# Kernel optimization log

Hardware: AMD Instinct MI355X
Metric: run time of the kernel (lower is better)

Reference implementation:

```python
import jax, jax.numpy as jnp
import numpy as np

E, B, C, M, H = 8, 2, 1024, 2048, 7168


def setup_inputs() -> dict:
    key = jax.random.key(0)
    k1, k2, k3, k4 = jax.random.split(key, 4)
    # kaiming_uniform-ish scale for weights (bound = sqrt(6/fan_in)/sqrt(1+5) ~ 1/sqrt(fan_in))
    s_in = 1.0 / np.sqrt(M)
    s_ffn = 1.0 / np.sqrt(H)
    return {
        "dispatch_input": jax.random.normal(k1, (E, B, C, M), dtype=jnp.float32),
        "w1": jax.random.uniform(k2, (E, M, H), dtype=jnp.float32, minval=-s_in, maxval=s_in),
        "w2": jax.random.uniform(k3, (E, H, M), dtype=jnp.float32, minval=-s_ffn, maxval=s_ffn),
        "w3": jax.random.uniform(k4, (E, M, H), dtype=jnp.float32, minval=-s_in, maxval=s_in),
    }


def reference(dispatch_input, w1, w2, w3):
    # Batched per-expert SwiGLU MLP.
    # gate: [E,B,C,H], up: [E,B,C,H]
    gate = jnp.einsum("ebcm,emh->ebch", dispatch_input, w1)
    up = jnp.einsum("ebcm,emh->ebch", dispatch_input, w3)
    hidden = jax.nn.silu(gate) * up
    out = jnp.einsum("ebch,ehm->ebcm", hidden, w2)
    return out
```

## Files before the change

kernel.cpp:

```cpp
#include <hip/hip_runtime.h>

typedef __attribute__((ext_vector_type(8))) short bf16x8;
typedef __attribute__((ext_vector_type(4))) float f32x4;
typedef __attribute__((ext_vector_type(4))) unsigned int u32x4;
typedef __attribute__((ext_vector_type(4))) unsigned short u16x4;

#define NE 8
#define NT 2048
#define NM 2048
#define NH 7168

#define BAR() asm volatile("s_barrier" ::: "memory")
#define WAITV(N) asm volatile("s_waitcnt vmcnt(" #N ")" ::: "memory")

__device__ __forceinline__ unsigned short f2bf(float f) {
    unsigned int u = __float_as_uint(f);
    return (unsigned short)((u + 0x7fffu + ((u >> 16) & 1u)) >> 16);
}

__device__ __forceinline__ void gld16(const void* g, void* l) {
    __builtin_amdgcn_global_load_lds(
        (const __attribute__((address_space(1))) void*)g,
        (__attribute__((address_space(3))) void*)l, 16, 0, 0);
}


__global__ __launch_bounds__(256) void convert_x_kernel(
        const float* __restrict__ in, unsigned short* __restrict__ out) {
    const int i = blockIdx.x * 256 + threadIdx.x;
    f32x4 a = ((const f32x4*)in)[i];
    ((u16x4*)out)[i] = (u16x4){f2bf(a[0]), f2bf(a[1]), f2bf(a[2]), f2bf(a[3])};
}

__global__ __launch_bounds__(256) void convert_wT_kernel(
        const float* __restrict__ in, unsigned short* __restrict__ out,
        int R, int C) {
    const int t = threadIdx.x;
    const int e = blockIdx.y;
    const int tiles_c = C >> 6;
    const int tr = blockIdx.x / tiles_c, tc = blockIdx.x % tiles_c;

    const float* ip = in + (size_t)e * R * C + (size_t)(tr * 64) * C + tc * 64;
    unsigned short* op = out + (size_t)e * R * C + (size_t)(tc * 64) * R + tr * 64;

    __shared__ unsigned short tl[64][68];

    const int rr = t >> 4, c4 = (t & 15) * 4;
#pragma unroll
    for (int q = 0; q < 4; ++q) {
        const int r = q * 16 + rr;
        f32x4 v = *(const f32x4*)(ip + (size_t)r * C + c4);
        *(u16x4*)&tl[r][c4] = (u16x4){f2bf(v[0]), f2bf(v[1]), f2bf(v[2]), f2bf(v[3])};
    }
    __syncthreads();
#pragma unroll
    for (int q = 0; q < 4; ++q) {
        const int oc = q * 16 + rr;
        u16x4 v = (u16x4){tl[c4][oc], tl[c4 + 1][oc], tl[c4 + 2][oc], tl[c4 + 3][oc]};
        *(u16x4*)(op + (size_t)oc * R + c4) = v;
    }
}

__global__ __launch_bounds__(256) void convert_w13_kernel(
        const float* __restrict__ w1, const float* __restrict__ w3,
        unsigned short* __restrict__ wcat) {
    const int t = threadIdx.x;
    const int e = blockIdx.y;
    const int tiles_c = NH >> 6;
    const int tr = blockIdx.x / tiles_c, tc = blockIdx.x % tiles_c;

    __shared__ unsigned short tl[64][68];
    const int rr = t >> 4, c4 = (t & 15) * 4;
    unsigned short* ob = wcat + (size_t)e * (2 * NH) * NM + (size_t)(tc * 128) * NM + tr * 64;

#pragma unroll
    for (int pass = 0; pass < 2; ++pass) {
        const float* ip = (pass ? w3 : w1) + (size_t)e * NM * NH + (size_t)(tr * 64) * NH + tc * 64;
        if (pass) __syncthreads();
#pragma unroll
        for (int q = 0; q < 4; ++q) {
            const int r = q * 16 + rr;
            f32x4 v = *(const f32x4*)(ip + (size_t)r * NH + c4);
            *(u16x4*)&tl[r][c4] = (u16x4){f2bf(v[0]), f2bf(v[1]), f2bf(v[2]), f2bf(v[3])};
        }
        __syncthreads();
#pragma unroll
        for (int q = 0; q < 4; ++q) {
            const int oc = q * 16 + rr;
            const int orow = ((oc >> 4) * 32) + pass * 16 + (oc & 15);
            u16x4 v = (u16x4){tl[c4][oc], tl[c4 + 1][oc], tl[c4 + 2][oc], tl[c4 + 3][oc]};
            *(u16x4*)(ob + (size_t)orow * NM + c4) = v;
        }
    }
}

__global__ __launch_bounds__(512, 2) void gemm1p_kernel(
        const unsigned short* __restrict__ xb, const unsigned short* __restrict__ wcat,
        unsigned short* __restrict__ hid) {
    const int tid = threadIdx.x;
    const int lane = tid & 63, wv = tid >> 6;
    const int wr = wv >> 2, wc = wv & 3;
    const int e = blockIdx.y;
    const int d = blockIdx.x;
    const int l = (d & 7) * 56 + (d >> 3);
    const int ct = l >> 3, tt = l & 7;

    const unsigned short* ag = xb   + (size_t)(e * NT + tt * 256) * NM;
    const unsigned short* bg = wcat + (size_t)e * (2 * NH) * NM + (size_t)(ct * 256) * NM;
    unsigned short* hg = hid + (size_t)(e * NT + tt * 256) * NH + ct * 128;

    __shared__ __align__(16) unsigned short lds[2 * 16384];

    const int frow = lane & 15;
    const int fks  = (lane >> 4) * 8;
    const int la   = lane * 8;
    const int lr   = lane & 15, lq = lane >> 4;

    f32x4 acc[8][4];
#pragma unroll
    for (int m = 0; m < 8; ++m)
#pragma unroll
        for (int n = 0; n < 4; ++n) acc[m][n] = (f32x4){0.f, 0.f, 0.f, 0.f};

    auto stageA = [&](int t, int buf) {
        unsigned short* dst = lds + buf * 16384 + wv * 512;
        const unsigned short* src = ag + (size_t)(wv * 16 + frow) * NM + t * 32 + fks;
        gld16(src, dst);
        gld16(src + (size_t)128 * NM, dst + 8 * 512);
    };
    auto stageB = [&](int t, int buf) {
        unsigned short* dst = lds + buf * 16384 + 8192 + wv * 512;
        const unsigned short* src = bg + (size_t)(wv * 16 + frow) * NM + t * 32 + fks;
        gld16(src, dst);
        gld16(src + (size_t)128 * NM, dst + 8 * 512);
    };

    auto body = [&](int buf) {
        const unsigned short* bA = lds + buf * 16384;
        const unsigned short* bB = bA + 8192;
        bf16x8 af[4], bf[4];
#pragma unroll
        for (int m = 0; m < 4; ++m)
            af[m] = *(const bf16x8*)(bA + (wr * 8 + m) * 512 + la);
#pragma unroll
        for (int n = 0; n < 4; ++n)
            bf[n] = *(const bf16x8*)(bB + (wc * 4 + n) * 512 + la);
        __builtin_amdgcn_s_setprio(1);
#pragma unroll
        for (int m = 0; m < 4; ++m)
#pragma unroll
            for (int n = 0; n < 4; ++n)
                acc[m][n] = __builtin_amdgcn_mfma_f32_16x16x32_bf16(af[m], bf[n], acc[m][n], 0, 0, 0);
        __builtin_amdgcn_s_setprio(0);
#pragma unroll
        for (int m = 0; m < 4; ++m)
            af[m] = *(const bf16x8*)(bA + (wr * 8 + 4 + m) * 512 + la);
        __builtin_amdgcn_s_setprio(1);
#pragma unroll
        for (int m = 0; m < 4; ++m)
#pragma unroll
            for (int n = 0; n < 4; ++n)
                acc[4 + m][n] = __builtin_amdgcn_mfma_f32_16x16x32_bf16(af[m], bf[n], acc[4 + m][n], 0, 0, 0);
        __builtin_amdgcn_s_setprio(0);
    };

    const int NKT = NM / 32;
    stageA(0, 0); stageB(0, 0);

    int buf = 0;
    for (int t = 0; t < NKT; ++t) {
        if (t + 1 < NKT) {
            stageA(t + 1, buf ^ 1);
            stageB(t + 1, buf ^ 1);
            WAITV(4);
        } else {
            WAITV(0);
        }
        BAR();
        body(buf);
        BAR();
        buf ^= 1;
    }

#pragma unroll
    for (int mf = 0; mf < 8; ++mf)
#pragma unroll
        for (int p = 0; p < 2; ++p)
#pragma unroll
            for (int i = 0; i < 4; ++i) {
                const float g = acc[mf][2 * p][i];
                const float u = acc[mf][2 * p + 1][i];
                const float s = g / (1.f + __expf(-g));
                const int r = wr * 128 + mf * 16 + lq * 4 + i;
                const int h = wc * 32 + p * 16 + lr;
                hg[(size_t)r * NH + h] = f2bf(s * u);
            }
}

__global__ __launch_bounds__(512, 2) void gemm2p_kernel(
        const unsigned short* __restrict__ hid, const unsigned short* __restrict__ w2t,
        float* __restrict__ out) {
    const int tid = threadIdx.x;
    const int lane = tid & 63, wv = tid >> 6;
    const int wr = wv >> 2, wc = wv & 3;
    const int e = blockIdx.y;
    const int d = blockIdx.x;
    const int l = (d & 7) * 8 + (d >> 3);
    const int mt = l >> 3, tt = l & 7;

    const unsigned short* ag = hid + (size_t)(e * NT + tt * 256) * NH;
    const unsigned short* bg = w2t + (size_t)e * NM * NH + (size_t)(mt * 256) * NH;
    float* og = out + (size_t)(e * NT + tt * 256) * NM + mt * 256;

    __shared__ __align__(16) unsigned short lds[2 * 16384];

    const int frow = lane & 15;
    const int fks  = (lane >> 4) * 8;
    const int la   = lane * 8;
    const int lr   = lane & 15, lq = lane >> 4;

    f32x4 acc[8][4];
#pragma unroll
    for (int m = 0; m < 8; ++m)
#pragma unroll
        for (int n = 0; n < 4; ++n) acc[m][n] = (f32x4){0.f, 0.f, 0.f, 0.f};

    auto stageA = [&](int t, int buf) {
        unsigned short* dst = lds + buf * 16384 + wv * 512;
        const unsigned short* src = ag + (size_t)(wv * 16 + frow) * NH + t * 32 + fks;
        gld16(src, dst);
        gld16(src + (size_t)128 * NH, dst + 8 * 512);
    };
    auto stageB = [&](int t, int buf) {
        unsigned short* dst = lds + buf * 16384 + 8192 + wv * 512;
        const unsigned short* src = bg + (size_t)(wv * 16 + frow) * NH + t * 32 + fks;
        gld16(src, dst);
        gld16(src + (size_t)128 * NH, dst + 8 * 512);
    };

    auto body = [&](int buf) {
        const unsigned short* bA = lds + buf * 16384;
        const unsigned short* bB = bA + 8192;
        bf16x8 af[4], bf[4];
#pragma unroll
        for (int m = 0; m < 4; ++m)
            af[m] = *(const bf16x8*)(bA + (wr * 8 + m) * 512 + la);
#pragma unroll
        for (int n = 0; n < 4; ++n)
            bf[n] = *(const bf16x8*)(bB + (wc * 4 + n) * 512 + la);
        __builtin_amdgcn_s_setprio(1);
#pragma unroll
        for (int m = 0; m < 4; ++m)
#pragma unroll
            for (int n = 0; n < 4; ++n)
                acc[m][n] = __builtin_amdgcn_mfma_f32_16x16x32_bf16(af[m], bf[n], acc[m][n], 0, 0, 0);
        __builtin_amdgcn_s_setprio(0);
#pragma unroll
        for (int m = 0; m < 4; ++m)
            af[m] = *(const bf16x8*)(bA + (wr * 8 + 4 + m) * 512 + la);
        __builtin_amdgcn_s_setprio(1);
#pragma unroll
        for (int m = 0; m < 4; ++m)
#pragma unroll
            for (int n = 0; n < 4; ++n)
                acc[4 + m][n] = __builtin_amdgcn_mfma_f32_16x16x32_bf16(af[m], bf[n], acc[4 + m][n], 0, 0, 0);
        __builtin_amdgcn_s_setprio(0);
    };

    const int NKT = NH / 32;
    stageA(0, 0); stageB(0, 0);

    int buf = 0;
    for (int t = 0; t < NKT; ++t) {
        if (t + 1 < NKT) {
            stageA(t + 1, buf ^ 1);
            stageB(t + 1, buf ^ 1);
            WAITV(4);
        } else {
            WAITV(0);
        }
        BAR();
        body(buf);
        BAR();
        buf ^= 1;
    }

#pragma unroll
    for (int mf = 0; mf < 8; ++mf)
#pragma unroll
        for (int n = 0; n < 4; ++n)
#pragma unroll
            for (int i = 0; i < 4; ++i) {
                const int r = wr * 128 + mf * 16 + lq * 4 + i;
                const int c = wc * 64 + n * 16 + lr;
                og[(size_t)r * NM + c] = acc[mf][n][i];
            }
}

#define ROWB 80
#define TILEB (128 * ROWB)

__global__ __launch_bounds__(256, 2) void gemm1_fb_kernel(
        const float* __restrict__ x, const float* __restrict__ w1,
        const float* __restrict__ w3, unsigned short* __restrict__ hid) {
    const int tid = threadIdx.x;
    const int e = blockIdx.y;
    const int d = blockIdx.x;
    const int l = (d & 7) * 112 + (d >> 3);
    const int hn = l >> 4, tm = l & 15;

    const float* xg  = x  + (size_t)(e * NT + tm * 128) * NM;
    const float* w1g = w1 + (size_t)e * NM * NH + hn * 128;
    const float* w3g = w3 + (size_t)e * NM * NH + hn * 128;
    unsigned short* hg = hid + (size_t)(e * NT + tm * 128) * NH + hn * 128;

    __shared__ __align__(16) unsigned char lds[2 * 3 * TILEB];

    const int a_r = tid >> 3, a_c4 = tid & 7;
    const int w_kq = (tid >> 2) & 7;
    const int w_cg = ((tid >> 5) << 2) | (tid & 3);

    const int lane = tid & 63;
    const int wv = tid >> 6;
    const int r0w = (wv >> 1) * 64, c0w = (wv & 1) * 64;
    const int lr = lane & 15, lq = lane >> 4;

    f32x4 accg[4][4], accu[4][4];
#pragma unroll
    for (int m = 0; m < 4; ++m)
#pragma unroll
        for (int n = 0; n < 4; ++n) {
            accg[m][n] = (f32x4){0.f, 0.f, 0.f, 0.f};
            accu[m][n] = (f32x4){0.f, 0.f, 0.f, 0.f};
        }

    f32x4 la0, la1, la2, la3;
    f32x4 l10, l11, l12, l13, l30, l31, l32, l33;

    auto stage_load = [&](int ks) {
        const int k0 = ks * 32;
        const float* pa = xg + (size_t)a_r * NM + k0 + a_c4 * 4;
        la0 = *(const f32x4*)(pa);
        la1 = *(const f32x4*)(pa + 32 * NM);
        la2 = *(const f32x4*)(pa + 64 * NM);
        la3 = *(const f32x4*)(pa + 96 * NM);
        const float* p1 = w1g + (size_t)(k0 + w_kq * 4) * NH + w_cg * 4;
        l10 = *(const f32x4*)(p1);
        l11 = *(const f32x4*)(p1 + NH);
        l12 = *(const f32x4*)(p1 + 2 * NH);
        l13 = *(const f32x4*)(p1 + 3 * NH);
        const float* p3 = w3g + (size_t)(k0 + w_kq * 4) * NH + w_cg * 4;
        l30 = *(const f32x4*)(p3);
        l31 = *(const f32x4*)(p3 + NH);
        l32 = *(const f32x4*)(p3 + 2 * NH);
        l33 = *(const f32x4*)(p3 + 3 * NH);
    };

    auto stage_write = [&](int buf) {
        unsigned char* base = lds + buf * (3 * TILEB);
        unsigned char* pa = base + a_r * ROWB + a_c4 * 8;
        *(u16x4*)(pa)             = (u16x4){f2bf(la0[0]), f2bf(la0[1]), f2bf(la0[2]), f2bf(la0[3])};
        *(u16x4*)(pa + 32 * ROWB) = (u16x4){f2bf(la1[0]), f2bf(la1[1]), f2bf(la1[2]), f2bf(la1[3])};
        *(u16x4*)(pa + 64 * ROWB) = (u16x4){f2bf(la2[0]), f2bf(la2[1]), f2bf(la2[2]), f2bf(la2[3])};
        *(u16x4*)(pa + 96 * ROWB) = (u16x4){f2bf(la3[0]), f2bf(la3[1]), f2bf(la3[2]), f2bf(la3[3])};
        unsigned char* pw1 = base + TILEB + w_kq * 8;
#pragma unroll
        for (int j = 0; j < 4; ++j) {
            const int c = w_cg * 4 + j;
            *(u16x4*)(pw1 + c * ROWB) =
                (u16x4){f2bf(l10[j]), f2bf(l11[j]), f2bf(l12[j]), f2bf(l13[j])};
        }
        unsigned char* pw3 = base + 2 * TILEB + w_kq * 8;
#pragma unroll
        for (int j = 0; j < 4; ++j) {
            const int c = w_cg * 4 + j;
            *(u16x4*)(pw3 + c * ROWB) =
                (u16x4){f2bf(l30[j]), f2bf(l31[j]), f2bf(l32[j]), f2bf(l33[j])};
        }
    };

    auto compute = [&](int buf) {
        const unsigned char* base = lds + buf * (3 * TILEB);
        bf16x8 af[4], b1f[4], b3f[4];
#pragma unroll
        for (int m = 0; m < 4; ++m)
            af[m] = *(const bf16x8*)(base + (r0w + m * 16 + lr) * ROWB + lq * 16);
#pragma unroll
        for (int n = 0; n < 4; ++n) {
            b1f[n] = *(const bf16x8*)(base + TILEB + (c0w + n * 16 + lr) * ROWB + lq * 16);
            b3f[n] = *(const bf16x8*)(base + 2 * TILEB + (c0w + n * 16 + lr) * ROWB + lq * 16);
        }
#pragma unroll
        for (int m = 0; m < 4; ++m)
#pragma unroll
            for (int n = 0; n < 4; ++n) {
                accg[m][n] = __builtin_amdgcn_mfma_f32_16x16x32_bf16(af[m], b1f[n], accg[m][n], 0, 0, 0);
                accu[m][n] = __builtin_amdgcn_mfma_f32_16x16x32_bf16(af[m], b3f[n], accu[m][n], 0, 0, 0);
            }
    };

    stage_load(0);
    stage_write(0);
    __syncthreads();
    int cur = 0;
    const int NK = NM / 32;
    for (int ks = 0; ks < NK; ++ks) {
        const bool more = (ks + 1 < NK);
        if (more) stage_load(ks + 1);
        compute(cur);
        if (more) {
            stage_write(cur ^ 1);
            __syncthreads();
        }
        cur ^= 1;
    }

#pragma unroll
    for (int m = 0; m < 4; ++m)
#pragma unroll
        for (int n = 0; n < 4; ++n)
#pragma unroll
            for (int i = 0; i < 4; ++i) {
                const float g = accg[m][n][i];
                const float u = accu[m][n][i];
                const float s = g / (1.f + __expf(-g));
                const int r = r0w + m * 16 + lq * 4 + i;
                const int c = c0w + n * 16 + lr;
                hg[(size_t)r * NH + c] = f2bf(s * u);
            }
}

__global__ __launch_bounds__(256, 2) void gemm2_fb_kernel(
        const unsigned short* __restrict__ hid, const float* __restrict__ w2,
        float* __restrict__ out) {
    const int tid = threadIdx.x;
    const int e = blockIdx.y;
    const int d = blockIdx.x;
    const int l = (d & 7) * 32 + (d >> 3);
    const int mn = l >> 4, tm = l & 15;

    const unsigned short* ag = hid + (size_t)(e * NT + tm * 128) * NH;
    const float* wg = w2 + (size_t)e * NH * NM + mn * 128;
    float* og = out + (size_t)(e * NT + tm * 128) * NM + mn * 128;

    __shared__ __align__(16) unsigned char lds[2 * 2 * TILEB];

    const int a_row = tid >> 2, a_ch = tid & 3;
    const int w_kq = (tid >> 2) & 7;
    const int w_cg = ((tid >> 5) << 2) | (tid & 3);

    const int lane = tid & 63;
    const int wv = tid >> 6;
    const int r0w = (wv >> 1) * 64, c0w = (wv & 1) * 64;
    const int lr = lane & 15, lq = lane >> 4;

    f32x4 acc[4][4];
#pragma unroll
    for (int m = 0; m < 4; ++m)
#pragma unroll
        for (int n = 0; n < 4; ++n) acc[m][n] = (f32x4){0.f, 0.f, 0.f, 0.f};

    u32x4 lau0, lau1;
    f32x4 lw0, lw1, lw2, lw3;

    auto stage_load = [&](int ks) {
        const int k0 = ks * 32;
        lau0 = *(const u32x4*)(ag + (size_t)a_row * NH + k0 + a_ch * 8);
        lau1 = *(const u32x4*)(ag + (size_t)(a_row + 64) * NH + k0 + a_ch * 8);
        const float* p = wg + (size_t)(k0 + w_kq * 4) * NM + w_cg * 4;
        lw0 = *(const f32x4*)(p);
        lw1 = *(const f32x4*)(p + NM);
        lw2 = *(const f32x4*)(p + 2 * NM);
        lw3 = *(const f32x4*)(p + 3 * NM);
    };

    auto stage_write = [&](int buf) {
        unsigned char* base = lds + buf * (2 * TILEB);
        *(u32x4*)(base + a_row * ROWB + a_ch * 16) = lau0;
        *(u32x4*)(base + (a_row + 64) * ROWB + a_ch * 16) = lau1;
        unsigned char* pw = base + TILEB + w_kq * 8;
#pragma unroll
        for (int j = 0; j < 4; ++j) {
            const int c = w_cg * 4 + j;
            *(u16x4*)(pw + c * ROWB) =
                (u16x4){f2bf(lw0[j]), f2bf(lw1[j]), f2bf(lw2[j]), f2bf(lw3[j])};
        }
    };

    auto compute = [&](int buf) {
        const unsigned char* base = lds + buf * (2 * TILEB);
        bf16x8 af[4], bf[4];
#pragma unroll
        for (int m = 0; m < 4; ++m)
            af[m] = *(const bf16x8*)(base + (r0w + m * 16 + lr) * ROWB + lq * 16);
#pragma unroll
        for (int n = 0; n < 4; ++n)
            bf[n] = *(const bf16x8*)(base + TILEB + (c0w + n * 16 + lr) * ROWB + lq * 16);
#pragma unroll
        for (int m = 0; m < 4; ++m)
#pragma unroll
            for (int n = 0; n < 4; ++n)
                acc[m][n] = __builtin_amdgcn_mfma_f32_16x16x32_bf16(af[m], bf[n], acc[m][n], 0, 0, 0);
    };

    stage_load(0);
    stage_write(0);
    __syncthreads();
    int cur = 0;
    const int NK = NH / 32;
    for (int ks = 0; ks < NK; ++ks) {
        const bool more = (ks + 1 < NK);
        if (more) stage_load(ks + 1);
        compute(cur);
        if (more) {
            stage_write(cur ^ 1);
            __syncthreads();
        }
        cur ^= 1;
    }

#pragma unroll
    for (int m = 0; m < 4; ++m)
#pragma unroll
        for (int n = 0; n < 4; ++n)
#pragma unroll
            for (int i = 0; i < 4; ++i) {
                const int r = r0w + m * 16 + lq * 4 + i;
                const int c = c0w + n * 16 + lr;
                og[(size_t)r * NM + c] = acc[m][n][i];
            }
}


extern "C" void kernel_launch(void* const* d_in, const int* in_sizes, int n_in,
                              void* d_out, int out_size, void* d_ws, size_t ws_size,
                              hipStream_t stream) {
    const float* x  = (const float*)d_in[0];
    const float* w1 = (const float*)d_in[1];
    const float* w2 = (const float*)d_in[2];
    const float* w3 = (const float*)d_in[3];
    float* out = (float*)d_out;

    const size_t XB_SZ   = (size_t)NE * NT * NM * 2;
    const size_t WCAT_SZ = (size_t)NE * 2 * NH * NM * 2;
    const size_t HID_SZ  = (size_t)NE * NT * NH * 2;
    const size_t NEED = XB_SZ + WCAT_SZ + HID_SZ;

    if (ws_size >= NEED) {
        unsigned char* ws = (unsigned char*)d_ws;
        unsigned short* xbp  = (unsigned short*)(ws);
        unsigned short* wcat = (unsigned short*)(ws + XB_SZ);
        unsigned short* hidb = (unsigned short*)(ws + XB_SZ + WCAT_SZ);
        unsigned short* w2t  = (unsigned short*)(ws);

        convert_x_kernel<<<dim3((NE * NT * NM) / 1024), 256, 0, stream>>>(x, xbp);
        convert_w13_kernel<<<dim3((NM / 64) * (NH / 64), NE), 256, 0, stream>>>(w1, w3, wcat);
        gemm1p_kernel<<<dim3(448, NE), 512, 0, stream>>>(xbp, wcat, hidb);
        convert_wT_kernel<<<dim3((NH / 64) * (NM / 64), NE), 256, 0, stream>>>(w2, w2t, NH, NM);
        gemm2p_kernel<<<dim3(64, NE), 512, 0, stream>>>(hidb, w2t, out);
    } else {
        unsigned short* hid = (unsigned short*)d_ws;
        gemm1_fb_kernel<<<dim3(896, NE), 256, 0, stream>>>(x, w1, w3, hid);
        gemm2_fb_kernel<<<dim3(256, NE), 256, 0, stream>>>(hid, w2, out);
    }
}
```

Baseline: 2.009 ms.

## Deepen K-tile to 64 and interleave prefetch with MFMA phases in both GEMMs

Both the gate/up GEMM and the down-projection GEMM now stage a 64-wide K slice per double buffer instead of 32, which doubles the LDS footprint to 128 KB per block. The loop is split into four MFMA phases, and each phase issues one quarter of the next tile's global-to-LDS loads. Barriers and partial vmcnt waits sit between the phases, so loads overlap compute at a finer grain and per-iteration barrier overhead is amortized over twice the K. The larger LDS use at launch bounds (512,2) risks lowering occupancy to one block per CU, and the loop now has more barriers per iteration.

```diff
diff --git a/kernel.cpp b/kernel.cpp
--- a/kernel.cpp
+++ b/kernel.cpp
@@ -109,7 +109,7 @@
     const unsigned short* bg = wcat + (size_t)e * (2 * NH) * NM + (size_t)(ct * 256) * NM;
     unsigned short* hg = hid + (size_t)(e * NT + tt * 256) * NH + ct * 128;
 
-    __shared__ __align__(16) unsigned short lds[2 * 16384];
+    __shared__ __align__(16) unsigned short lds[2 * 32768];
 
     const int frow = lane & 15;
     const int fks  = (lane >> 4) * 8;
@@ -122,64 +122,87 @@
 #pragma unroll
         for (int n = 0; n < 4; ++n) acc[m][n] = (f32x4){0.f, 0.f, 0.f, 0.f};
 
-    auto stageA = [&](int t, int buf) {
-        unsigned short* dst = lds + buf * 16384 + wv * 512;
-        const unsigned short* src = ag + (size_t)(wv * 16 + frow) * NM + t * 32 + fks;
+    auto stageA = [&](int t, int kh, int buf) {
+        unsigned short* dst = lds + buf * 32768 + (kh * 16 + wv) * 512;
+        const unsigned short* src = ag + (size_t)(wv * 16 + frow) * NM + t * 64 + kh * 32 + fks;
         gld16(src, dst);
         gld16(src + (size_t)128 * NM, dst + 8 * 512);
     };
-    auto stageB = [&](int t, int buf) {
-        unsigned short* dst = lds + buf * 16384 + 8192 + wv * 512;
-        const unsigned short* src = bg + (size_t)(wv * 16 + frow) * NM + t * 32 + fks;
+    auto stageB = [&](int t, int kh, int buf) {
+        unsigned short* dst = lds + buf * 32768 + 16384 + (kh * 16 + wv) * 512;
+        const unsigned short* src = bg + (size_t)(wv * 16 + frow) * NM + t * 64 + kh * 32 + fks;
         gld16(src, dst);
         gld16(src + (size_t)128 * NM, dst + 8 * 512);
     };
 
-    auto body = [&](int buf) {
-        const unsigned short* bA = lds + buf * 16384;
-        const unsigned short* bB = bA + 8192;
-        bf16x8 af[4], bf[4];
-#pragma unroll
-        for (int m = 0; m < 4; ++m)
-            af[m] = *(const bf16x8*)(bA + (wr * 8 + m) * 512 + la);
-#pragma unroll
-        for (int n = 0; n < 4; ++n)
-            bf[n] = *(const bf16x8*)(bB + (wc * 4 + n) * 512 + la);
-        __builtin_amdgcn_s_setprio(1);
-#pragma unroll
-        for (int m = 0; m < 4; ++m)
-#pragma unroll
-            for (int n = 0; n < 4; ++n)
-                acc[m][n] = __builtin_amdgcn_mfma_f32_16x16x32_bf16(af[m], bf[n], acc[m][n], 0, 0, 0);
-        __builtin_amdgcn_s_setprio(0);
-#pragma unroll
-        for (int m = 0; m < 4; ++m)
-            af[m] = *(const bf16x8*)(bA + (wr * 8 + 4 + m) * 512 + la);
-        __builtin_amdgcn_s_setprio(1);
-#pragma unroll
-        for (int m = 0; m < 4; ++m)
-#pragma unroll
-            for (int n = 0; n < 4; ++n)
-                acc[4 + m][n] = __builtin_amdgcn_mfma_f32_16x16x32_bf16(af[m], bf[n], acc[4 + m][n], 0, 0, 0);
-        __builtin_amdgcn_s_setprio(0);
-    };
-
-    const int NKT = NM / 32;
-    stageA(0, 0); stageB(0, 0);
-
-    int buf = 0;
+    const int NKT = NM / 64;
+    stageA(0, 0, 0); stageB(0, 0, 0); stageA(0, 1, 0); stageB(0, 1, 0);
+    WAITV(4); BAR();
+
     for (int t = 0; t < NKT; ++t) {
-        if (t + 1 < NKT) {
-            stageA(t + 1, buf ^ 1);
-            stageB(t + 1, buf ^ 1);
-            WAITV(4);
-        } else {
-            WAITV(0);
-        }
-        BAR();
-        body(buf);
-        BAR();
-        buf ^= 1;
+        const int buf = t & 1, nb = buf ^ 1;
+        const bool more = (t + 1 < NKT);
+        const unsigned short* bA = lds + buf * 32768;
+        const unsigned short* bB = bA + 16384;
+        bf16x8 af[4], bfr[4];
+
+#pragma unroll
+        for (int m = 0; m < 4; ++m) af[m] = *(const bf16x8*)(bA + (wr * 8 + m) * 512 + la);
+#pragma unroll
+        for (int n = 0; n < 4; ++n) bfr[n] = *(const bf16x8*)(bB + (wc * 4 + n) * 512 + la);
+        if (more) stageA(t + 1, 0, nb);
+        BAR();
+        __builtin_amdgcn_s_setprio(1);
+#pragma unroll
+        for (int m = 0; m < 4; ++m)
+#pragma unroll
+            for (int n = 0; n < 4; ++n)
+                acc[m][n] = __builtin_amdgcn_mfma_f32_16x16x32_bf16(af[m], bfr[n], acc[m][n], 0, 0, 0);
+        __builtin_amdgcn_s_setprio(0);
+        BAR();
+
+#pragma unroll
+        for (int m = 0; m < 4; ++m) af[m] = *(const bf16x8*)(bA + (wr * 8 + 4 + m) * 512 + la);
+        if (more) stageB(t + 1, 0, nb);
+        BAR();
+        __builtin_amdgcn_s_setprio(1);
+#pragma unroll
+        for (int m = 0; m < 4; ++m)
+#pragma unroll
+            for (int n = 0; n < 4; ++n)
+                acc[4 + m][n] = __builtin_amdgcn_mfma_f32_16x16x32_bf16(af[m], bfr[n], acc[4 + m][n], 0, 0, 0);
+        __builtin_amdgcn_s_setprio(0);
+        if (more) { WAITV(4); } else { WAITV(0); }
+        BAR();
+
+#pragma unroll
+        for (int m = 0; m < 4; ++m) af[m] = *(const bf16x8*)(bA + (16 + wr * 8 + m) * 512 + la);
+#pragma unroll
+        for (int n = 0; n < 4; ++n) bfr[n] = *(const bf16x8*)(bB + (16 + wc * 4 + n) * 512 + la);
+        if (more) stageA(t + 1, 1, nb);
+        BAR();
+        __builtin_amdgcn_s_setprio(1);
+#pragma unroll
+        for (int m = 0; m < 4; ++m)
+#pragma unroll
+            for (int n = 0; n < 4; ++n)
+                acc[m][n] = __builtin_amdgcn_mfma_f32_16x16x32_bf16(af[m], bfr[n], acc[m][n], 0, 0, 0);
+        __builtin_amdgcn_s_setprio(0);
+        BAR();
+
+#pragma unroll
+        for (int m = 0; m < 4; ++m) af[m] = *(const bf16x8*)(bA + (16 + wr * 8 + 4 + m) * 512 + la);
+        if (more) stageB(t + 1, 1, nb);
+        BAR();
+        __builtin_amdgcn_s_setprio(1);
+#pragma unroll
+        for (int m = 0; m < 4; ++m)
+#pragma unroll
+            for (int n = 0; n < 4; ++n)
+                acc[4 + m][n] = __builtin_amdgcn_mfma_f32_16x16x32_bf16(af[m], bfr[n], acc[4 + m][n], 0, 0, 0);
+        __builtin_amdgcn_s_setprio(0);
+        if (more) { WAITV(4); }
+        BAR();
     }
 
 #pragma unroll
@@ -212,7 +235,7 @@
     const unsigned short* bg = w2t + (size_t)e * NM * NH + (size_t)(mt * 256) * NH;
     float* og = out + (size_t)(e * NT + tt * 256) * NM + mt * 256;
 
-    __shared__ __align__(16) unsigned short lds[2 * 16384];
+    __shared__ __align__(16) unsigned short lds[2 * 32768];
 
     const int frow = lane & 15;
     const int fks  = (lane >> 4) * 8;
@@ -225,64 +248,87 @@
 #pragma unroll
         for (int n = 0; n < 4; ++n) acc[m][n] = (f32x4){0.f, 0.f, 0.f, 0.f};
 
-    auto stageA = [&](int t, int buf) {
-        unsigned short* dst = lds + buf * 16384 + wv * 512;
-        const unsigned short* src = ag + (size_t)(wv * 16 + frow) * NH + t * 32 + fks;
+    auto stageA = [&](int t, int kh, int buf) {
+        unsigned short* dst = lds + buf * 32768 + (kh * 16 + wv) * 512;
+        const unsigned short* src = ag + (size_t)(wv * 16 + frow) * NH + t * 64 + kh * 32 + fks;
         gld16(src, dst);
         gld16(src + (size_t)128 * NH, dst + 8 * 512);
     };
-    auto stageB = [&](int t, int buf) {
-        unsigned short* dst = lds + buf * 16384 + 8192 + wv * 512;
-        const unsigned short* src = bg + (size_t)(wv * 16 + frow) * NH + t * 32 + fks;
+    auto stageB = [&](int t, int kh, int buf) {
+        unsigned short* dst = lds + buf * 32768 + 16384 + (kh * 16 + wv) * 512;
+        const unsigned short* src = bg + (size_t)(wv * 16 + frow) * NH + t * 64 + kh * 32 + fks;
         gld16(src, dst);
         gld16(src + (size_t)128 * NH, dst + 8 * 512);
     };
 
-    auto body = [&](int buf) {
-        const unsigned short* bA = lds + buf * 16384;
-        const unsigned short* bB = bA + 8192;
-        bf16x8 af[4], bf[4];
-#pragma unroll
-        for (int m = 0; m < 4; ++m)
-            af[m] = *(const bf16x8*)(bA + (wr * 8 + m) * 512 + la);
-#pragma unroll
-        for (int n = 0; n < 4; ++n)
-            bf[n] = *(const bf16x8*)(bB + (wc * 4 + n) * 512 + la);
-        __builtin_amdgcn_s_setprio(1);
-#pragma unroll
-        for (int m = 0; m < 4; ++m)
-#pragma unroll
-            for (int n = 0; n < 4; ++n)
-                acc[m][n] = __builtin_amdgcn_mfma_f32_16x16x32_bf16(af[m], bf[n], acc[m][n], 0, 0, 0);
-        __builtin_amdgcn_s_setprio(0);
-#pragma unroll
-        for (int m = 0; m < 4; ++m)
-            af[m] = *(const bf16x8*)(bA + (wr * 8 + 4 + m) * 512 + la);
-        __builtin_amdgcn_s_setprio(1);
-#pragma unroll
-        for (int m = 0; m < 4; ++m)
-#pragma unroll
-            for (int n = 0; n < 4; ++n)
-                acc[4 + m][n] = __builtin_amdgcn_mfma_f32_16x16x32_bf16(af[m], bf[n], acc[4 + m][n], 0, 0, 0);
-        __builtin_amdgcn_s_setprio(0);
-    };
-
-    const int NKT = NH / 32;
-    stageA(0, 0); stageB(0, 0);
-
-    int buf = 0;
+    const int NKT = NH / 64;
+    stageA(0, 0, 0); stageB(0, 0, 0); stageA(0, 1, 0); stageB(0, 1, 0);
+    WAITV(4); BAR();
+
     for (int t = 0; t < NKT; ++t) {
-        if (t + 1 < NKT) {
-            stageA(t + 1, buf ^ 1);
-            stageB(t + 1, buf ^ 1);
-            WAITV(4);
-        } else {
-            WAITV(0);
-        }
-        BAR();
-        body(buf);
-        BAR();
-        buf ^= 1;
+        const int buf = t & 1, nb = buf ^ 1;
+        const bool more = (t + 1 < NKT);
+        const unsigned short* bA = lds + buf * 32768;
+        const unsigned short* bB = bA + 16384;
+        bf16x8 af[4], bfr[4];
+
+#pragma unroll
+        for (int m = 0; m < 4; ++m) af[m] = *(const bf16x8*)(bA + (wr * 8 + m) * 512 + la);
+#pragma unroll
+        for (int n = 0; n < 4; ++n) bfr[n] = *(const bf16x8*)(bB + (wc * 4 + n) * 512 + la);
+        if (more) stageA(t + 1, 0, nb);
+        BAR();
+        __builtin_amdgcn_s_setprio(1);
+#pragma unroll
+        for (int m = 0; m < 4; ++m)
+#pragma unroll
+            for (int n = 0; n < 4; ++n)
+                acc[m][n] = __builtin_amdgcn_mfma_f32_16x16x32_bf16(af[m], bfr[n], acc[m][n], 0, 0, 0);
+        __builtin_amdgcn_s_setprio(0);
+        BAR();
+
+#pragma unroll
+        for (int m = 0; m < 4; ++m) af[m] = *(const bf16x8*)(bA + (wr * 8 + 4 + m) * 512 + la);
+        if (more) stageB(t + 1, 0, nb);
+        BAR();
+        __builtin_amdgcn_s_setprio(1);
+#pragma unroll
+        for (int m = 0; m < 4; ++m)
+#pragma unroll
+            for (int n = 0; n < 4; ++n)
+                acc[4 + m][n] = __builtin_amdgcn_mfma_f32_16x16x32_bf16(af[m], bfr[n], acc[4 + m][n], 0, 0, 0);
+        __builtin_amdgcn_s_setprio(0);
+        if (more) { WAITV(4); } else { WAITV(0); }
+        BAR();
+
+#pragma unroll
+        for (int m = 0; m < 4; ++m) af[m] = *(const bf16x8*)(bA + (16 + wr * 8 + m) * 512 + la);
+#pragma unroll
+        for (int n = 0; n < 4; ++n) bfr[n] = *(const bf16x8*)(bB + (16 + wc * 4 + n) * 512 + la);
+        if (more) stageA(t + 1, 1, nb);
+        BAR();
+        __builtin_amdgcn_s_setprio(1);
+#pragma unroll
+        for (int m = 0; m < 4; ++m)
+#pragma unroll
+            for (int n = 0; n < 4; ++n)
+                acc[m][n] = __builtin_amdgcn_mfma_f32_16x16x32_bf16(af[m], bfr[n], acc[m][n], 0, 0, 0);
+        __builtin_amdgcn_s_setprio(0);
+        BAR();
+
+#pragma unroll
+        for (int m = 0; m < 4; ++m) af[m] = *(const bf16x8*)(bA + (16 + wr * 8 + 4 + m) * 512 + la);
+        if (more) stageB(t + 1, 1, nb);
+        BAR();
+        __builtin_amdgcn_s_setprio(1);
+#pragma unroll
+        for (int m = 0; m < 4; ++m)
+#pragma unroll
+            for (int n = 0; n < 4; ++n)
+                acc[4 + m][n] = __builtin_amdgcn_mfma_f32_16x16x32_bf16(af[m], bfr[n], acc[4 + m][n], 0, 0, 0);
+        __builtin_amdgcn_s_setprio(0);
+        if (more) { WAITV(4); }
+        BAR();
     }
 
 #pragma unroll
```

Measured after the change: 1.952 ms. -2.8%, faster.
